# Kernel tuning notes

Measured on AMD Instinct MI355X. Metric: run time of the kernel, lower is better.

## Reference

```python
import jax, jax.numpy as jnp
import numpy as np

# Model dims (match init_kwargs)
D_MODEL = 1024
D_INNER = 2048
D_STATE = 16
D_CONV = 4
DT_RANK = 64
H = 8                      # num_heads
P = D_INNER // H           # head_dim = 256
DT_MIN, DT_MAX = 1e-4, 1.0
BATCH, SEQ = 2, 4096
TOTAL_OUT = 2 * D_INNER + DT_RANK + 2 * H * D_STATE  # 4416 (no gated delta)
EPS = 1e-6


def _xavier(k, shape):
    fan_out, fan_in = shape
    return jax.random.normal(k, shape, jnp.float32) * np.sqrt(2.0 / (fan_in + fan_out))


def setup_inputs() -> dict:
    key = jax.random.key(0)
    ks = jax.random.split(key, 8)
    x = jax.random.normal(ks[0], (BATCH, SEQ, D_MODEL), jnp.float32)
    W_in = _xavier(ks[1], (TOTAL_OUT, D_MODEL))          # in_proj (no bias)
    W_dt = _xavier(ks[2], (H, DT_RANK))                  # dt_proj (no bias)
    conv_w = jax.random.normal(ks[3], (D_INNER, D_CONV), jnp.float32) * 0.1
    conv_b = jnp.zeros((D_INNER,), jnp.float32)
    # A_log init: log(1..d_state) per head
    A_log = jnp.broadcast_to(jnp.log(jnp.arange(1, D_STATE + 1, dtype=jnp.float32)), (H, D_STATE))
    Dskip = jnp.ones((H, P), jnp.float32)
    # dt_bias = inverse_softplus(dt), dt log-uniform in [dt_min, dt_max]
    dt0 = jnp.exp(jax.random.uniform(ks[4], (H,), jnp.float32)
                  * (np.log(DT_MAX) - np.log(DT_MIN)) + np.log(DT_MIN))
    dt_bias = dt0 + jnp.log(-jnp.expm1(-dt0))
    norm_w = jnp.ones((D_INNER,), jnp.float32)
    W_out = _xavier(ks[5], (D_MODEL, D_INNER))
    W_res = _xavier(ks[6], (D_INNER, D_MODEL))           # residual_proj (d_model != d_inner)
    return dict(x=x, W_in=W_in, W_dt=W_dt, conv_w=conv_w, conv_b=conv_b,
                A_log=A_log, Dskip=Dskip, dt_bias=dt_bias, norm_w=norm_w,
                W_out=W_out, W_res=W_res)


def _causal_dwconv(u, w, b):
    # u: (B,L,C) -> causal depthwise conv along L. w: (C,K), b: (C,)
    lhs = u.transpose(0, 2, 1)               # (B,C,L)
    rhs = w[:, None, :]                      # (C,1,K)
    out = jax.lax.conv_general_dilated(
        lhs, rhs, window_strides=(1,), padding=[(D_CONV - 1, 0)],
        dimension_numbers=('NCH', 'OIH', 'NCH'), feature_group_count=D_INNER)
    return (out + b[None, :, None]).transpose(0, 2, 1)


def reference(x, W_in, W_dt, conv_w, conv_b, A_log, Dskip, dt_bias, norm_w, W_out, W_res):
    Bsz, L, _ = x.shape
    p = x @ W_in.T                                            # (B,L,TOTAL_OUT)
    splits = np.cumsum([D_INNER, D_INNER, DT_RANK, H * D_STATE]).tolist()
    z, u, dt_h, Bf, Cf = jnp.split(p, splits, axis=-1)
    Bp = Bf.reshape(Bsz, L, H, D_STATE)
    Cp = Cf.reshape(Bsz, L, H, D_STATE)
    u = _causal_dwconv(u, conv_w, conv_b)                     # (B,L,D_INNER)
    # dt_prep: softplus(dt_raw + bias) clamped to [dt_min, dt_max]
    dt = jnp.clip(jax.nn.softplus(dt_h @ W_dt.T + dt_bias), DT_MIN, DT_MAX)  # (B,L,H)
    A = -jnp.exp(A_log)                                       # (H,N)
    uh = u.reshape(Bsz, L, H, P)

    def step(h, inp):
        u_t, dt_t, B_t, C_t = inp                             # (B,H,P),(B,H),(B,H,N),(B,H,N)
        dA = jnp.exp(dt_t[..., None] * A)                     # (B,H,N)
        h = h * dA[:, :, None, :] + (dt_t[:, :, None, None] * u_t[..., None]) * B_t[:, :, None, :]
        y_t = jnp.einsum('bhpn,bhn->bhp', h, C_t)
        return h, y_t

    h0 = jnp.zeros((Bsz, H, P, D_STATE), x.dtype)
    xs = (uh.transpose(1, 0, 2, 3), dt.transpose(1, 0, 2),
          Bp.transpose(1, 0, 2, 3), Cp.transpose(1, 0, 2, 3))
    _, ys = jax.lax.scan(step, h0, xs)                        # (L,B,H,P)
    y = ys.transpose(1, 0, 2, 3) + Dskip[None, None] * uh     # skip connection
    y = y.reshape(Bsz, L, D_INNER)

    residual_inner = x @ W_res.T                              # residual_proj
    # fused_out: g = RMSNorm(y * silu(z) + residual) * weight
    g = y * jax.nn.silu(z) + residual_inner
    g = g * jax.lax.rsqrt(jnp.mean(g * g, axis=-1, keepdims=True) + EPS) * norm_w
    return g @ W_out.T
```

## Files before the change

kernel.cpp:

```cpp
#include <hip/hip_runtime.h>
#include <hip/hip_bf16.h>
#include <math.h>

#define DMODEL  1024
#define DINNER  2048
#define DSTATE  16
#define DCONV   4
#define DTRANK  64
#define NH      8
#define PH      256
#define TOTOUT  4416
#define NPAD    4608
#define NTOT    6656
#define MB_ROWS 4096
#define LC      64
#define NCB     (MB_ROWS/LC)

typedef __attribute__((ext_vector_type(8))) short bf16x8;
typedef __attribute__((ext_vector_type(4))) float f32x4;

__device__ inline unsigned cvt2bf(float lo, float hi) {
    unsigned r;
    asm("v_cvt_pk_bf16_f32 %0, %1, %2" : "=v"(r) : "v"(lo), "v"(hi));
    return r;
}
__device__ inline ushort f2bf(float v) { return (ushort)(cvt2bf(v, v) & 0xffffu); }
__device__ inline float bf2f(ushort u) {
    union { unsigned u; float f; } w; w.u = (unsigned)u << 16; return w.f;
}
__device__ inline void gload16(const ushort* g, ushort* l) {
    __builtin_amdgcn_global_load_lds((const __attribute__((address_space(1))) unsigned*)(const void*)g,
                                     (__attribute__((address_space(3))) unsigned*)(void*)l, 16, 0, 0);
}

__global__ __launch_bounds__(256) void cvt_bf(const float* __restrict__ s,
                                              ushort* __restrict__ d) {
    size_t i = ((size_t)blockIdx.x * 256 + threadIdx.x) * 8;
    float4 v0 = *(const float4*)(s + i);
    float4 v1 = *(const float4*)(s + i + 4);
    uint4 o;
    o.x = cvt2bf(v0.x, v0.y); o.y = cvt2bf(v0.z, v0.w);
    o.z = cvt2bf(v1.x, v1.y); o.w = cvt2bf(v1.z, v1.w);
    *(uint4*)(d + i) = o;
}

__global__ __launch_bounds__(256) void cvt_weights(const float* __restrict__ W_in,
                                                   const float* __restrict__ W_res,
                                                   const float* __restrict__ W_out,
                                                   ushort* __restrict__ dst) {
    const size_t E0 = (size_t)TOTOUT * DMODEL;
    const size_t E1 = (size_t)NPAD * DMODEL;
    const size_t E2 = (size_t)NTOT * DMODEL;
    size_t i = ((size_t)blockIdx.x * 256 + threadIdx.x) * 8;
    float4 v0, v1;
    if (i < E1) {
        if (i < E0) { v0 = *(const float4*)(W_in + i); v1 = *(const float4*)(W_in + i + 4); }
        else { v0 = make_float4(0.f,0.f,0.f,0.f); v1 = v0; }
    } else if (i < E2) {
        size_t o = i - E1; v0 = *(const float4*)(W_res + o); v1 = *(const float4*)(W_res + o + 4);
    } else {
        size_t o = i - E2; v0 = *(const float4*)(W_out + o); v1 = *(const float4*)(W_out + o + 4);
    }
    uint4 o;
    o.x = cvt2bf(v0.x, v0.y); o.y = cvt2bf(v0.z, v0.w);
    o.z = cvt2bf(v1.x, v1.y); o.w = cvt2bf(v1.z, v1.w);
    *(uint4*)(dst + i) = o;
}

__global__ __launch_bounds__(512, 2) void gemm_big(const ushort* __restrict__ A,
                                                   const ushort* __restrict__ W,
                                                   ushort* __restrict__ Zb,
                                                   ushort* __restrict__ Ub,
                                                   float* __restrict__ DBCp,
                                                   ushort* __restrict__ RESb,
                                                   int ntx, int K) {
    __shared__ __align__(16) ushort L[3 * 16384];
    const int nwg  = gridDim.x;
    const int orig = blockIdx.x;
    const int swz  = (orig & 7) * (nwg >> 3) + (orig >> 3);
    const int bx = swz % ntx, by = swz / ntx;
    const int row0 = by * 256, col0 = bx * 256;

    const int t    = threadIdx.x;
    const int lane = t & 63, w = t >> 6;
    const int wr   = w >> 2, wc = w & 3;
    const int l15  = lane & 15, l4 = lane >> 4;

    const int r0g = t >> 2, s0g = t & 3;
    const int r1g = r0g + 128;
    const int rr0 = r0g ^ ((r0g >> 3) & 1), cc0 = s0g ^ ((r0g >> 1) & 3);
    const int rr1 = r1g ^ ((r1g >> 3) & 1), cc1 = s0g ^ ((r1g >> 1) & 3);
    const ushort* sA0 = A + (size_t)(row0 + rr0) * K + cc0 * 8;
    const ushort* sA1 = A + (size_t)(row0 + rr1) * K + cc1 * 8;
    const ushort* sB0 = W + (size_t)(col0 + rr0) * K + cc0 * 8;
    const ushort* sB1 = W + (size_t)(col0 + rr1) * K + cc1 * 8;

    int offA[8], offB[4];
    #pragma unroll
    for (int mi = 0; mi < 8; mi++) {
        int r = wr * 128 + mi * 16 + l15;
        offA[mi] = (r * 32 + l4 * 8) ^ (((r >> 1) & 7) << 3);
    }
    #pragma unroll
    for (int ni = 0; ni < 4; ni++) {
        int r = wc * 64 + ni * 16 + l15;
        offB[ni] = 8192 + ((r * 32 + l4 * 8) ^ (((r >> 1) & 7) << 3));
    }

    f32x4 acc[8][4];
    #pragma unroll
    for (int i = 0; i < 8; i++)
        #pragma unroll
        for (int j = 0; j < 4; j++)
            acc[i][j] = (f32x4){0.f, 0.f, 0.f, 0.f};

    const int KT = K >> 5;
    gload16(sA0,      &L[t * 8]);
    gload16(sA1,      &L[4096 + t * 8]);
    gload16(sB0,      &L[8192 + t * 8]);
    gload16(sB1,      &L[12288 + t * 8]);
    gload16(sA0 + 32, &L[16384 + t * 8]);
    gload16(sA1 + 32, &L[16384 + 4096 + t * 8]);
    gload16(sB0 + 32, &L[16384 + 8192 + t * 8]);
    gload16(sB1 + 32, &L[16384 + 12288 + t * 8]);
    asm volatile("s_waitcnt vmcnt(4)" ::: "memory");
    __builtin_amdgcn_sched_barrier(0);
    __builtin_amdgcn_s_barrier();
    __builtin_amdgcn_sched_barrier(0);

    for (int kt = 0; kt < KT; ++kt) {
        const bool pre = (kt + 2) < KT;
        if (pre) {
            ushort* bp2 = &L[((kt + 2) % 3) * 16384];
            const int ko = (kt + 2) << 5;
            gload16(sA0 + ko, bp2 + t * 8);
            gload16(sA1 + ko, bp2 + 4096 + t * 8);
            gload16(sB0 + ko, bp2 + 8192 + t * 8);
            gload16(sB1 + ko, bp2 + 12288 + t * 8);
        }
        const ushort* bp = &L[(kt % 3) * 16384];
        bf16x8 af[8], bw[4];
        #pragma unroll
        for (int mi = 0; mi < 8; mi++) af[mi] = *(const bf16x8*)(bp + offA[mi]);
        #pragma unroll
        for (int ni = 0; ni < 4; ni++) bw[ni] = *(const bf16x8*)(bp + offB[ni]);
        __builtin_amdgcn_s_setprio(1);
        #pragma unroll
        for (int mi = 0; mi < 8; mi++)
            #pragma unroll
            for (int ni = 0; ni < 4; ni++)
                acc[mi][ni] = __builtin_amdgcn_mfma_f32_16x16x32_bf16(af[mi], bw[ni], acc[mi][ni], 0, 0, 0);
        __builtin_amdgcn_s_setprio(0);
        if (pre) { asm volatile("s_waitcnt vmcnt(4)" ::: "memory"); }
        else     { asm volatile("s_waitcnt vmcnt(0)" ::: "memory"); }
        __builtin_amdgcn_sched_barrier(0);
        __builtin_amdgcn_s_barrier();
        __builtin_amdgcn_sched_barrier(0);
    }

    #pragma unroll
    for (int mi = 0; mi < 8; mi++) {
        #pragma unroll
        for (int ni = 0; ni < 4; ni++) {
            #pragma unroll
            for (int r = 0; r < 4; r++) {
                const int row = row0 + wr * 128 + mi * 16 + l4 * 4 + r;
                const int col = col0 + wc * 64 + ni * 16 + l15;
                const float v = acc[mi][ni][r];
                if (col0 < DINNER) {
                    Zb[(size_t)row * DINNER + col] = f2bf(v);
                } else if (col0 < 2 * DINNER) {
                    Ub[(size_t)row * DINNER + (col - DINNER)] = f2bf(v);
                } else if (col0 < NPAD) {
                    if (col < TOTOUT)
                        DBCp[(size_t)row * 320 + (col - 2 * DINNER)] = v;
                } else {
                    RESb[(size_t)row * DINNER + (col - NPAD)] = f2bf(v);
                }
            }
        }
    }
}

__global__ __launch_bounds__(512) void gemm_out(const ushort* __restrict__ A,
                                                const ushort* __restrict__ W,
                                                float* __restrict__ C0,
                                                int ntx, int K, int ldc) {
    __shared__ __align__(16) ushort L[3 * 12288];
    const int nwg  = gridDim.x;
    const int orig = blockIdx.x;
    const int swz  = (orig & 7) * (nwg >> 3) + (orig >> 3);
    const int bx = swz % ntx, by = swz / ntx;
    const int row0 = by * 256, col0 = bx * 128;

    const int t    = threadIdx.x;
    const int lane = t & 63, w = t >> 6;
    const int wr   = w >> 1, wc = w & 1;
    const int l15  = lane & 15, l4 = lane >> 4;

    const int r0g = t >> 2, s0g = t & 3;
    const int r1g = r0g + 128;
    const int rr0 = r0g ^ ((r0g >> 3) & 1), cc0 = s0g ^ ((r0g >> 1) & 3);
    const int rr1 = r1g ^ ((r1g >> 3) & 1), cc1 = s0g ^ ((r1g >> 1) & 3);
    const ushort* sA0 = A + (size_t)(row0 + rr0) * K + cc0 * 8;
    const ushort* sA1 = A + (size_t)(row0 + rr1) * K + cc1 * 8;
    const ushort* sB0 = W + (size_t)(col0 + rr0) * K + cc0 * 8;

    int offA[4], offB[4];
    #pragma unroll
    for (int mi = 0; mi < 4; mi++) {
        int r = wr * 64 + mi * 16 + l15;
        offA[mi] = (r * 32 + l4 * 8) ^ (((r >> 1) & 7) << 3);
    }
    #pragma unroll
    for (int ni = 0; ni < 4; ni++) {
        int r = wc * 64 + ni * 16 + l15;
        offB[ni] = 8192 + ((r * 32 + l4 * 8) ^ (((r >> 1) & 7) << 3));
    }

    f32x4 acc[4][4];
    #pragma unroll
    for (int i = 0; i < 4; i++)
        #pragma unroll
        for (int j = 0; j < 4; j++)
            acc[i][j] = (f32x4){0.f, 0.f, 0.f, 0.f};

    const int KT = K >> 5;
    gload16(sA0,      &L[t * 8]);
    gload16(sA1,      &L[4096 + t * 8]);
    gload16(sB0,      &L[8192 + t * 8]);
    gload16(sA0 + 32, &L[12288 + t * 8]);
    gload16(sA1 + 32, &L[12288 + 4096 + t * 8]);
    gload16(sB0 + 32, &L[12288 + 8192 + t * 8]);
    asm volatile("s_waitcnt vmcnt(3)" ::: "memory");
    __builtin_amdgcn_sched_barrier(0);
    __builtin_amdgcn_s_barrier();
    __builtin_amdgcn_sched_barrier(0);

    for (int kt = 0; kt < KT; ++kt) {
        const bool pre = (kt + 2) < KT;
        if (pre) {
            ushort* bp2 = &L[((kt + 2) % 3) * 12288];
            const int ko = (kt + 2) << 5;
            gload16(sA0 + ko, bp2 + t * 8);
            gload16(sA1 + ko, bp2 + 4096 + t * 8);
            gload16(sB0 + ko, bp2 + 8192 + t * 8);
        }
        const ushort* bp = &L[(kt % 3) * 12288];
        bf16x8 af[4], bw[4];
        #pragma unroll
        for (int mi = 0; mi < 4; mi++) af[mi] = *(const bf16x8*)(bp + offA[mi]);
        #pragma unroll
        for (int ni = 0; ni < 4; ni++) bw[ni] = *(const bf16x8*)(bp + offB[ni]);
        __builtin_amdgcn_s_setprio(1);
        #pragma unroll
        for (int mi = 0; mi < 4; mi++)
            #pragma unroll
            for (int ni = 0; ni < 4; ni++)
                acc[mi][ni] = __builtin_amdgcn_mfma_f32_16x16x32_bf16(af[mi], bw[ni], acc[mi][ni], 0, 0, 0);
        __builtin_amdgcn_s_setprio(0);
        if (pre) { asm volatile("s_waitcnt vmcnt(3)" ::: "memory"); }
        else     { asm volatile("s_waitcnt vmcnt(0)" ::: "memory"); }
        __builtin_amdgcn_sched_barrier(0);
        __builtin_amdgcn_s_barrier();
        __builtin_amdgcn_sched_barrier(0);
    }

    #pragma unroll
    for (int mi = 0; mi < 4; mi++)
        #pragma unroll
        for (int ni = 0; ni < 4; ni++)
            #pragma unroll
            for (int r = 0; r < 4; r++) {
                const int row = row0 + wr * 64 + mi * 16 + l4 * 4 + r;
                const int col = col0 + wc * 64 + ni * 16 + l15;
                C0[(size_t)row * ldc + col] = acc[mi][ni][r];
            }
}

__global__ __launch_bounds__(256) void dt_kernel(const float* __restrict__ DBC,
                                                 const float* __restrict__ W_dt,
                                                 const float* __restrict__ dt_bias,
                                                 const float* __restrict__ A_log,
                                                 float* __restrict__ dt,
                                                 float* __restrict__ dA) {
    int idx = blockIdx.x * blockDim.x + threadIdx.x;
    int h = idx % NH;
    int tr = idx / NH;
    const float* row = DBC + (size_t)tr * 320;
    float acc = dt_bias[h];
    #pragma unroll
    for (int r = 0; r < DTRANK; r++) acc = fmaf(row[r], W_dt[h * DTRANK + r], acc);
    float sp = acc > 20.f ? acc : log1pf(expf(acc));
    sp = fminf(fmaxf(sp, 1e-4f), 1.0f);
    dt[idx] = sp;
    #pragma unroll
    for (int n = 0; n < DSTATE; n++)
        dA[(size_t)idx * DSTATE + n] = expf(sp * (-expf(A_log[h * DSTATE + n])));
}

__global__ __launch_bounds__(256) void scan_local(const ushort* __restrict__ Ub,
                                                  const float* __restrict__ DBC,
                                                  const float* __restrict__ dt_,
                                                  const float* __restrict__ dA_,
                                                  const float* __restrict__ cw,
                                                  const float* __restrict__ cb,
                                                  float* __restrict__ hloc,
                                                  float* __restrict__ Pc) {
    const int c = blockIdx.x, h = blockIdx.y;
    const int pidx = threadIdx.x;
    const int ch = h * PH + pidx;
    const int t0 = c * LC;
    __shared__ float sdA[LC][DSTATE];
    __shared__ float sdB[LC][DSTATE];
    const int st = pidx >> 4, sn = pidx & 15;
    #pragma unroll
    for (int j = 0; j < 4; j++) {
        int tt = st + j * 16;
        size_t trow = (size_t)(t0 + tt);
        float dv = dt_[trow * NH + h];
        sdA[tt][sn] = dA_[(trow * NH + h) * DSTATE + sn];
        sdB[tt][sn] = dv * DBC[trow * 320 + 64 + h * DSTATE + sn];
    }
    const float w0 = cw[ch * 4], w1 = cw[ch * 4 + 1], w2 = cw[ch * 4 + 2], w3 = cw[ch * 4 + 3];
    const float bia = cb[ch];
    const int bs = (c / NCB) * MB_ROWS;
    float um3 = (t0 - 3 >= bs) ? bf2f(Ub[(size_t)(t0 - 3) * DINNER + ch]) : 0.f;
    float um2 = (t0 - 2 >= bs) ? bf2f(Ub[(size_t)(t0 - 2) * DINNER + ch]) : 0.f;
    float um1 = (t0 - 1 >= bs) ? bf2f(Ub[(size_t)(t0 - 1) * DINNER + ch]) : 0.f;
    __syncthreads();

    float hst[DSTATE] = {};
    for (int t = 0; t < LC; t++) {
        float u0 = bf2f(Ub[(size_t)(t0 + t) * DINNER + ch]);
        float up = fmaf(w3, u0, fmaf(w2, um1, fmaf(w1, um2, fmaf(w0, um3, bia))));
        um3 = um2; um2 = um1; um1 = u0;
        #pragma unroll
        for (int n = 0; n < DSTATE; n++)
            hst[n] = fmaf(hst[n], sdA[t][n], up * sdB[t][n]);
    }
    float* hl = hloc + (((size_t)c * NH + h) * PH + pidx) * DSTATE;
    #pragma unroll
    for (int n = 0; n < DSTATE; n++) hl[n] = hst[n];

    if (pidx < DSTATE) {
        float pr = 1.f;
        for (int t = 0; t < LC; t++) pr *= sdA[t][pidx];
        Pc[((size_t)c * NH + h) * DSTATE + pidx] = pr;
    }
}

__global__ __launch_bounds__(256) void scan_carry(const float* __restrict__ hloc,
                                                  const float* __restrict__ Pc,
                                                  float* __restrict__ Hent) {
    int g = blockIdx.x * 256 + threadIdx.x;
    int b = g >> 15;
    int r = g & 32767;
    int h = r >> 12;
    int inner = r & 4095;
    int n = r & 15;
    float carry = 0.f;
    for (int i = 0; i < NCB; i++) {
        int c = b * NCB + i;
        size_t idx = ((size_t)c * NH + h) * (PH * DSTATE) + inner;
        Hent[idx] = carry;
        carry = fmaf(Pc[((size_t)c * NH + h) * DSTATE + n], carry, hloc[idx]);
    }
}

__global__ __launch_bounds__(256) void scan_out(const ushort* __restrict__ Zb,
                                                const ushort* __restrict__ Ub,
                                                const ushort* __restrict__ RESb,
                                                ushort* __restrict__ Yb,
                                                const float* __restrict__ DBC,
                                                const float* __restrict__ dt_,
                                                const float* __restrict__ dA_,
                                                const float* __restrict__ cw,
                                                const float* __restrict__ cb,
                                                const float* __restrict__ Dskip,
                                                const float* __restrict__ Hent) {
    const int c = blockIdx.x, h = blockIdx.y;
    const int pidx = threadIdx.x;
    const int ch = h * PH + pidx;
    const int t0 = c * LC;
    __shared__ float sdA[LC][DSTATE];
    __shared__ float sdB[LC][DSTATE];
    __shared__ float sC [LC][DSTATE];
    const int st = pidx >> 4, sn = pidx & 15;
    #pragma unroll
    for (int j = 0; j < 4; j++) {
        int tt = st + j * 16;
        size_t trow = (size_t)(t0 + tt);
        float dv = dt_[trow * NH + h];
        sdA[tt][sn] = dA_[(trow * NH + h) * DSTATE + sn];
        sdB[tt][sn] = dv * DBC[trow * 320 + 64 + h * DSTATE + sn];
        sC [tt][sn] =      DBC[trow * 320 + 192 + h * DSTATE + sn];
    }
    const float w0 = cw[ch * 4], w1 = cw[ch * 4 + 1], w2 = cw[ch * 4 + 2], w3 = cw[ch * 4 + 3];
    const float bia = cb[ch];
    const int bs = (c / NCB) * MB_ROWS;
    float um3 = (t0 - 3 >= bs) ? bf2f(Ub[(size_t)(t0 - 3) * DINNER + ch]) : 0.f;
    float um2 = (t0 - 2 >= bs) ? bf2f(Ub[(size_t)(t0 - 2) * DINNER + ch]) : 0.f;
    float um1 = (t0 - 1 >= bs) ? bf2f(Ub[(size_t)(t0 - 1) * DINNER + ch]) : 0.f;
    const float dsk = Dskip[ch];
    float hst[DSTATE];
    const float* he = Hent + (((size_t)c * NH + h) * PH + pidx) * DSTATE;
    #pragma unroll
    for (int n = 0; n < DSTATE; n++) hst[n] = he[n];
    __syncthreads();

    for (int t = 0; t < LC; t++) {
        size_t off = (size_t)(t0 + t) * DINNER + ch;
        float u0 = bf2f(Ub[off]);
        float up = fmaf(w3, u0, fmaf(w2, um1, fmaf(w1, um2, fmaf(w0, um3, bia))));
        um3 = um2; um2 = um1; um1 = u0;
        float a0 = 0.f, a1 = 0.f, a2 = 0.f, a3 = 0.f;
        #pragma unroll
        for (int n = 0; n < 4; n++) {
            hst[n +  0] = fmaf(hst[n +  0], sdA[t][n +  0], up * sdB[t][n +  0]);
            hst[n +  4] = fmaf(hst[n +  4], sdA[t][n +  4], up * sdB[t][n +  4]);
            hst[n +  8] = fmaf(hst[n +  8], sdA[t][n +  8], up * sdB[t][n +  8]);
            hst[n + 12] = fmaf(hst[n + 12], sdA[t][n + 12], up * sdB[t][n + 12]);
            a0 = fmaf(hst[n +  0], sC[t][n +  0], a0);
            a1 = fmaf(hst[n +  4], sC[t][n +  4], a1);
            a2 = fmaf(hst[n +  8], sC[t][n +  8], a2);
            a3 = fmaf(hst[n + 12], sC[t][n + 12], a3);
        }
        float yv = ((a0 + a1) + (a2 + a3)) + dsk * up;
        float zv = bf2f(Zb[off]);
        float sil = zv / (1.f + expf(-zv));
        Yb[off] = f2bf(fmaf(yv, sil, bf2f(RESb[off])));
    }
}

__global__ __launch_bounds__(256) void rmsnorm_bf(const ushort* __restrict__ Yb,
                                                  const float* __restrict__ norm_w,
                                                  ushort* __restrict__ Gb) {
    const int row = blockIdx.x;
    const ushort* r = Yb + (size_t)row * DINNER;
    const int c0 = threadIdx.x * 8;
    uint4 packed = *(const uint4*)(r + c0);
    float v[8];
    v[0] = bf2f((ushort)(packed.x & 0xffff)); v[1] = bf2f((ushort)(packed.x >> 16));
    v[2] = bf2f((ushort)(packed.y & 0xffff)); v[3] = bf2f((ushort)(packed.y >> 16));
    v[4] = bf2f((ushort)(packed.z & 0xffff)); v[5] = bf2f((ushort)(packed.z >> 16));
    v[6] = bf2f((ushort)(packed.w & 0xffff)); v[7] = bf2f((ushort)(packed.w >> 16));
    float ss = 0.f;
    #pragma unroll
    for (int i = 0; i < 8; i++) ss = fmaf(v[i], v[i], ss);
    #pragma unroll
    for (int off = 32; off > 0; off >>= 1) ss += __shfl_down(ss, off);
    __shared__ float red[4];
    if ((threadIdx.x & 63) == 0) red[threadIdx.x >> 6] = ss;
    __syncthreads();
    float tot = red[0] + red[1] + red[2] + red[3];
    float inv = rsqrtf(tot / (float)DINNER + 1e-6f);
    float4 w0 = *(const float4*)(norm_w + c0);
    float4 w1 = *(const float4*)(norm_w + c0 + 4);
    uint4 o;
    o.x = cvt2bf(v[0] * inv * w0.x, v[1] * inv * w0.y);
    o.y = cvt2bf(v[2] * inv * w0.z, v[3] * inv * w0.w);
    o.z = cvt2bf(v[4] * inv * w1.x, v[5] * inv * w1.y);
    o.w = cvt2bf(v[6] * inv * w1.z, v[7] * inv * w1.w);
    *(uint4*)(Gb + (size_t)row * DINNER + c0) = o;
}

struct Lay {
    float *DBC, *DT, *DA, *PC, *HLOC, *HENT;
    ushort *YB, *ZB, *UB, *RESB, *XBF, *WB;
    size_t total;
};
static Lay mk_layout(char* base, int Mr) {
    size_t o = 0;
    auto take = [&](size_t bytes) { char* p = base + o; o = (o + bytes + 255) & ~(size_t)255; return p; };
    Lay l;
    l.YB   = (ushort*)take((size_t)Mr * 2048 * 2);
    l.DBC  = (float*) take((size_t)Mr * 320 * 4);
    l.DT   = (float*) take((size_t)Mr * 8 * 4);
    l.DA   = (float*) take((size_t)Mr * 128 * 4);
    l.PC   = (float*) take((size_t)(Mr / 64) * NH * DSTATE * 4);
    l.HLOC = (float*) take((size_t)Mr * 512 * 4);
    l.HENT = (float*) take((size_t)Mr * 512 * 4);
    l.ZB   = (ushort*)take((size_t)Mr * 2048 * 2);
    l.UB   = (ushort*)take((size_t)Mr * 2048 * 2);
    l.RESB = (ushort*)take((size_t)Mr * 2048 * 2);
    l.XBF  = (ushort*)take((size_t)8192 * 1024 * 2);
    l.WB   = (ushort*)take(((size_t)NTOT * 1024 + (size_t)1024 * 2048) * 2);
    l.total = o;
    return l;
}

extern "C" void kernel_launch(void* const* d_in, const int* in_sizes, int n_in,
                              void* d_out, int out_size, void* d_ws, size_t ws_size,
                              hipStream_t stream) {
    const float* x       = (const float*)d_in[0];
    const float* W_in    = (const float*)d_in[1];
    const float* W_dt    = (const float*)d_in[2];
    const float* conv_w  = (const float*)d_in[3];
    const float* conv_b  = (const float*)d_in[4];
    const float* A_log   = (const float*)d_in[5];
    const float* Dskip   = (const float*)d_in[6];
    const float* dt_bias = (const float*)d_in[7];
    const float* norm_w  = (const float*)d_in[8];
    const float* W_out   = (const float*)d_in[9];
    const float* W_res   = (const float*)d_in[10];
    float* out = (float*)d_out;

    Lay probe = mk_layout(nullptr, 2 * MB_ROWS);
    const bool fat = ws_size >= probe.total;
    const int Mr = fat ? 2 * MB_ROWS : MB_ROWS;
    const int npass = fat ? 1 : 2;
    const int nbc = fat ? 2 : 1;
    Lay l = mk_layout((char*)d_ws, Mr);

    ushort* wcat = l.WB;
    ushort* wotb = wcat + (size_t)NTOT * 1024;
    ushort* Gb   = l.ZB;

    cvt_weights<<<((NTOT * 1024 + 2048 * 1024) / 8) / 256, 256, 0, stream>>>(W_in, W_res, W_out, l.WB);
    cvt_bf<<<(2 * MB_ROWS * DMODEL / 8) / 256, 256, 0, stream>>>(x, l.XBF);

    for (int b = 0; b < npass; b++) {
        const ushort* xb = l.XBF + (size_t)b * MB_ROWS * DMODEL;
        float* outb = out + (size_t)b * MB_ROWS * DMODEL;
        const int nty = Mr / 256;

        gemm_big<<<26 * nty, 512, 0, stream>>>(xb, wcat, l.ZB, l.UB, l.DBC, l.RESB, 26, DMODEL);
        dt_kernel<<<(Mr * NH) / 256, 256, 0, stream>>>(l.DBC, W_dt, dt_bias, A_log, l.DT, l.DA);
        scan_local<<<dim3(Mr / LC, NH), 256, 0, stream>>>(l.UB, l.DBC, l.DT, l.DA, conv_w, conv_b, l.HLOC, l.PC);
        scan_carry<<<nbc * 128, 256, 0, stream>>>(l.HLOC, l.PC, l.HENT);
        scan_out<<<dim3(Mr / LC, NH), 256, 0, stream>>>(l.ZB, l.UB, l.RESB, l.YB, l.DBC, l.DT, l.DA,
                                                        conv_w, conv_b, Dskip, l.HENT);
        rmsnorm_bf<<<Mr, 256, 0, stream>>>(l.YB, norm_w, Gb);
        gemm_out<<<8 * nty, 512, 0, stream>>>(Gb, wotb, outb, 8, DINNER, DMODEL);
    }
}
```

Baseline: 326.4 us.

## Restructure big GEMM to BK=64 double-buffered pipeline with interleaved staged loads

Replaces the triple-buffered BK=32 main loop of the input-projection GEMM with a double-buffered BK=64 loop. Each K-step is split into four sub-phases, and each phase issues one quarter of the next tile's global loads before its MFMA block. The LDS layout changes to 16-element half-rows with a simple XOR swizzle, and the LDS footprint grows from 96KB to 128KB. The aim is to halve barrier count per K and overlap global loads with MFMA more finely. The cost is higher LDS use, which may limit 2 blocks per CU, and possible bank conflicts under the new swizzle.

```diff
diff --git a/kernel.cpp b/kernel.cpp
--- a/kernel.cpp
+++ b/kernel.cpp
@@ -67,14 +67,14 @@
     *(uint4*)(dst + i) = o;
 }
 
-__global__ __launch_bounds__(512, 2) void gemm_big(const ushort* __restrict__ A,
-                                                   const ushort* __restrict__ W,
-                                                   ushort* __restrict__ Zb,
-                                                   ushort* __restrict__ Ub,
-                                                   float* __restrict__ DBCp,
-                                                   ushort* __restrict__ RESb,
-                                                   int ntx, int K) {
-    __shared__ __align__(16) ushort L[3 * 16384];
+__global__ __launch_bounds__(512, 2) void gemm_big8(const ushort* __restrict__ A,
+                                                    const ushort* __restrict__ W,
+                                                    ushort* __restrict__ Zb,
+                                                    ushort* __restrict__ Ub,
+                                                    float* __restrict__ DBCp,
+                                                    ushort* __restrict__ RESb,
+                                                    int ntx, int K) {
+    __shared__ __align__(16) ushort L[2 * 32768];
     const int nwg  = gridDim.x;
     const int orig = blockIdx.x;
     const int swz  = (orig & 7) * (nwg >> 3) + (orig >> 3);
@@ -86,25 +86,26 @@
     const int wr   = w >> 2, wc = w & 3;
     const int l15  = lane & 15, l4 = lane >> 4;
 
-    const int r0g = t >> 2, s0g = t & 3;
-    const int r1g = r0g + 128;
-    const int rr0 = r0g ^ ((r0g >> 3) & 1), cc0 = s0g ^ ((r0g >> 1) & 3);
-    const int rr1 = r1g ^ ((r1g >> 3) & 1), cc1 = s0g ^ ((r1g >> 1) & 3);
-    const ushort* sA0 = A + (size_t)(row0 + rr0) * K + cc0 * 8;
-    const ushort* sA1 = A + (size_t)(row0 + rr1) * K + cc1 * 8;
-    const ushort* sB0 = W + (size_t)(col0 + rr0) * K + cc0 * 8;
-    const ushort* sB1 = W + (size_t)(col0 + rr1) * K + cc1 * 8;
+    const int r  = t >> 1, hp = t & 1;
+    const int kb = hp ^ ((r >> 2) & 1);
+    const ushort* sA = A + (size_t)(row0 + r) * K + kb * 8;
+    const ushort* sB = W + (size_t)(col0 + r) * K + kb * 8;
+    const int ldst = t * 8;
+
+#define STG(d, p, ko) do { \
+    gload16(sA + (ko) + (p) * 16, &L[(d) * 32768 + (p) * 4096 + ldst]); \
+    gload16(sB + (ko) + (p) * 16, &L[(d) * 32768 + 16384 + (p) * 4096 + ldst]); } while (0)
 
     int offA[8], offB[4];
     #pragma unroll
     for (int mi = 0; mi < 8; mi++) {
-        int r = wr * 128 + mi * 16 + l15;
-        offA[mi] = (r * 32 + l4 * 8) ^ (((r >> 1) & 7) << 3);
+        int R = wr * 128 + mi * 16 + l15;
+        offA[mi] = (l4 >> 1) * 4096 + R * 16 + (((l4 & 1) ^ ((R >> 2) & 1)) * 8);
     }
     #pragma unroll
     for (int ni = 0; ni < 4; ni++) {
-        int r = wc * 64 + ni * 16 + l15;
-        offB[ni] = 8192 + ((r * 32 + l4 * 8) ^ (((r >> 1) & 7) << 3));
+        int R = wc * 64 + ni * 16 + l15;
+        offB[ni] = 16384 + (l4 >> 1) * 4096 + R * 16 + (((l4 & 1) ^ ((R >> 2) & 1)) * 8);
     }
 
     f32x4 acc[8][4];
@@ -114,59 +115,135 @@
         for (int j = 0; j < 4; j++)
             acc[i][j] = (f32x4){0.f, 0.f, 0.f, 0.f};
 
-    const int KT = K >> 5;
-    gload16(sA0,      &L[t * 8]);
-    gload16(sA1,      &L[4096 + t * 8]);
-    gload16(sB0,      &L[8192 + t * 8]);
-    gload16(sB1,      &L[12288 + t * 8]);
-    gload16(sA0 + 32, &L[16384 + t * 8]);
-    gload16(sA1 + 32, &L[16384 + 4096 + t * 8]);
-    gload16(sB0 + 32, &L[16384 + 8192 + t * 8]);
-    gload16(sB1 + 32, &L[16384 + 12288 + t * 8]);
+    const int KT = K >> 6;
+    STG(0, 0, 0); STG(0, 1, 0); STG(0, 2, 0); STG(0, 3, 0);
     asm volatile("s_waitcnt vmcnt(4)" ::: "memory");
     __builtin_amdgcn_sched_barrier(0);
     __builtin_amdgcn_s_barrier();
     __builtin_amdgcn_sched_barrier(0);
 
     for (int kt = 0; kt < KT; ++kt) {
-        const bool pre = (kt + 2) < KT;
-        if (pre) {
-            ushort* bp2 = &L[((kt + 2) % 3) * 16384];
-            const int ko = (kt + 2) << 5;
-            gload16(sA0 + ko, bp2 + t * 8);
-            gload16(sA1 + ko, bp2 + 4096 + t * 8);
-            gload16(sB0 + ko, bp2 + 8192 + t * 8);
-            gload16(sB1 + ko, bp2 + 12288 + t * 8);
-        }
-        const ushort* bp = &L[(kt % 3) * 16384];
-        bf16x8 af[8], bw[4];
-        #pragma unroll
-        for (int mi = 0; mi < 8; mi++) af[mi] = *(const bf16x8*)(bp + offA[mi]);
-        #pragma unroll
-        for (int ni = 0; ni < 4; ni++) bw[ni] = *(const bf16x8*)(bp + offB[ni]);
+        const int d = kt & 1;
+        const bool pre = (kt + 1) < KT;
+        const int ko = (kt + 1) << 6;
+        const ushort* Lp = &L[d * 32768];
+        bf16x8 af0, af1, af2, af3, bw0, bw1, bw2, bw3;
+
+        if (pre) STG(d ^ 1, 0, ko);
+        bw0 = *(const bf16x8*)(Lp + offB[0]); bw1 = *(const bf16x8*)(Lp + offB[1]);
+        bw2 = *(const bf16x8*)(Lp + offB[2]); bw3 = *(const bf16x8*)(Lp + offB[3]);
+        af0 = *(const bf16x8*)(Lp + offA[0]); af1 = *(const bf16x8*)(Lp + offA[1]);
+        af2 = *(const bf16x8*)(Lp + offA[2]); af3 = *(const bf16x8*)(Lp + offA[3]);
         __builtin_amdgcn_s_setprio(1);
-        #pragma unroll
-        for (int mi = 0; mi < 8; mi++)
-            #pragma unroll
-            for (int ni = 0; ni < 4; ni++)
-                acc[mi][ni] = __builtin_amdgcn_mfma_f32_16x16x32_bf16(af[mi], bw[ni], acc[mi][ni], 0, 0, 0);
+        acc[0][0] = __builtin_amdgcn_mfma_f32_16x16x32_bf16(af0, bw0, acc[0][0], 0, 0, 0);
+        acc[0][1] = __builtin_amdgcn_mfma_f32_16x16x32_bf16(af0, bw1, acc[0][1], 0, 0, 0);
+        acc[0][2] = __builtin_amdgcn_mfma_f32_16x16x32_bf16(af0, bw2, acc[0][2], 0, 0, 0);
+        acc[0][3] = __builtin_amdgcn_mfma_f32_16x16x32_bf16(af0, bw3, acc[0][3], 0, 0, 0);
+        acc[1][0] = __builtin_amdgcn_mfma_f32_16x16x32_bf16(af1, bw0, acc[1][0], 0, 0, 0);
+        acc[1][1] = __builtin_amdgcn_mfma_f32_16x16x32_bf16(af1, bw1, acc[1][1], 0, 0, 0);
+        acc[1][2] = __builtin_amdgcn_mfma_f32_16x16x32_bf16(af1, bw2, acc[1][2], 0, 0, 0);
+        acc[1][3] = __builtin_amdgcn_mfma_f32_16x16x32_bf16(af1, bw3, acc[1][3], 0, 0, 0);
+        acc[2][0] = __builtin_amdgcn_mfma_f32_16x16x32_bf16(af2, bw0, acc[2][0], 0, 0, 0);
+        acc[2][1] = __builtin_amdgcn_mfma_f32_16x16x32_bf16(af2, bw1, acc[2][1], 0, 0, 0);
+        acc[2][2] = __builtin_amdgcn_mfma_f32_16x16x32_bf16(af2, bw2, acc[2][2], 0, 0, 0);
+        acc[2][3] = __builtin_amdgcn_mfma_f32_16x16x32_bf16(af2, bw3, acc[2][3], 0, 0, 0);
+        acc[3][0] = __builtin_amdgcn_mfma_f32_16x16x32_bf16(af3, bw0, acc[3][0], 0, 0, 0);
+        acc[3][1] = __builtin_amdgcn_mfma_f32_16x16x32_bf16(af3, bw1, acc[3][1], 0, 0, 0);
+        acc[3][2] = __builtin_amdgcn_mfma_f32_16x16x32_bf16(af3, bw2, acc[3][2], 0, 0, 0);
+        acc[3][3] = __builtin_amdgcn_mfma_f32_16x16x32_bf16(af3, bw3, acc[3][3], 0, 0, 0);
         __builtin_amdgcn_s_setprio(0);
+
+        if (pre) STG(d ^ 1, 1, ko);
+        af0 = *(const bf16x8*)(Lp + offA[4]); af1 = *(const bf16x8*)(Lp + offA[5]);
+        af2 = *(const bf16x8*)(Lp + offA[6]); af3 = *(const bf16x8*)(Lp + offA[7]);
+        __builtin_amdgcn_s_setprio(1);
+        acc[4][0] = __builtin_amdgcn_mfma_f32_16x16x32_bf16(af0, bw0, acc[4][0], 0, 0, 0);
+        acc[4][1] = __builtin_amdgcn_mfma_f32_16x16x32_bf16(af0, bw1, acc[4][1], 0, 0, 0);
+        acc[4][2] = __builtin_amdgcn_mfma_f32_16x16x32_bf16(af0, bw2, acc[4][2], 0, 0, 0);
+        acc[4][3] = __builtin_amdgcn_mfma_f32_16x16x32_bf16(af0, bw3, acc[4][3], 0, 0, 0);
+        acc[5][0] = __builtin_amdgcn_mfma_f32_16x16x32_bf16(af1, bw0, acc[5][0], 0, 0, 0);
+        acc[5][1] = __builtin_amdgcn_mfma_f32_16x16x32_bf16(af1, bw1, acc[5][1], 0, 0, 0);
+        acc[5][2] = __builtin_amdgcn_mfma_f32_16x16x32_bf16(af1, bw2, acc[5][2], 0, 0, 0);
+        acc[5][3] = __builtin_amdgcn_mfma_f32_16x16x32_bf16(af1, bw3, acc[5][3], 0, 0, 0);
+        acc[6][0] = __builtin_amdgcn_mfma_f32_16x16x32_bf16(af2, bw0, acc[6][0], 0, 0, 0);
+        acc[6][1] = __builtin_amdgcn_mfma_f32_16x16x32_bf16(af2, bw1, acc[6][1], 0, 0, 0);
+        acc[6][2] = __builtin_amdgcn_mfma_f32_16x16x32_bf16(af2, bw2, acc[6][2], 0, 0, 0);
+        acc[6][3] = __builtin_amdgcn_mfma_f32_16x16x32_bf16(af2, bw3, acc[6][3], 0, 0, 0);
+        acc[7][0] = __builtin_amdgcn_mfma_f32_16x16x32_bf16(af3, bw0, acc[7][0], 0, 0, 0);
+        acc[7][1] = __builtin_amdgcn_mfma_f32_16x16x32_bf16(af3, bw1, acc[7][1], 0, 0, 0);
+        acc[7][2] = __builtin_amdgcn_mfma_f32_16x16x32_bf16(af3, bw2, acc[7][2], 0, 0, 0);
+        acc[7][3] = __builtin_amdgcn_mfma_f32_16x16x32_bf16(af3, bw3, acc[7][3], 0, 0, 0);
+        __builtin_amdgcn_s_setprio(0);
+
         if (pre) { asm volatile("s_waitcnt vmcnt(4)" ::: "memory"); }
         else     { asm volatile("s_waitcnt vmcnt(0)" ::: "memory"); }
         __builtin_amdgcn_sched_barrier(0);
         __builtin_amdgcn_s_barrier();
         __builtin_amdgcn_sched_barrier(0);
-    }
+
+        if (pre) STG(d ^ 1, 2, ko);
+        bw0 = *(const bf16x8*)(Lp + 8192 + offB[0]); bw1 = *(const bf16x8*)(Lp + 8192 + offB[1]);
+        bw2 = *(const bf16x8*)(Lp + 8192 + offB[2]); bw3 = *(const bf16x8*)(Lp + 8192 + offB[3]);
+        af0 = *(const bf16x8*)(Lp + 8192 + offA[0]); af1 = *(const bf16x8*)(Lp + 8192 + offA[1]);
+        af2 = *(const bf16x8*)(Lp + 8192 + offA[2]); af3 = *(const bf16x8*)(Lp + 8192 + offA[3]);
+        __builtin_amdgcn_s_setprio(1);
+        acc[0][0] = __builtin_amdgcn_mfma_f32_16x16x32_bf16(af0, bw0, acc[0][0], 0, 0, 0);
+        acc[0][1] = __builtin_amdgcn_mfma_f32_16x16x32_bf16(af0, bw1, acc[0][1], 0, 0, 0);
+        acc[0][2] = __builtin_amdgcn_mfma_f32_16x16x32_bf16(af0, bw2, acc[0][2], 0, 0, 0);
+        acc[0][3] = __builtin_amdgcn_mfma_f32_16x16x32_bf16(af0, bw3, acc[0][3], 0, 0, 0);
+        acc[1][0] = __builtin_amdgcn_mfma_f32_16x16x32_bf16(af1, bw0, acc[1][0], 0, 0, 0);
+        acc[1][1] = __builtin_amdgcn_mfma_f32_16x16x32_bf16(af1, bw1, acc[1][1], 0, 0, 0);
+        acc[1][2] = __builtin_amdgcn_mfma_f32_16x16x32_bf16(af1, bw2, acc[1][2], 0, 0, 0);
+        acc[1][3] = __builtin_amdgcn_mfma_f32_16x16x32_bf16(af1, bw3, acc[1][3], 0, 0, 0);
+        acc[2][0] = __builtin_amdgcn_mfma_f32_16x16x32_bf16(af2, bw0, acc[2][0], 0, 0, 0);
+        acc[2][1] = __builtin_amdgcn_mfma_f32_16x16x32_bf16(af2, bw1, acc[2][1], 0, 0, 0);
+        acc[2][2] = __builtin_amdgcn_mfma_f32_16x16x32_bf16(af2, bw2, acc[2][2], 0, 0, 0);
+        acc[2][3] = __builtin_amdgcn_mfma_f32_16x16x32_bf16(af2, bw3, acc[2][3], 0, 0, 0);
+        acc[3][0] = __builtin_amdgcn_mfma_f32_16x16x32_bf16(af3, bw0, acc[3][0], 0, 0, 0);
+        acc[3][1] = __builtin_amdgcn_mfma_f32_16x16x32_bf16(af3, bw1, acc[3][1], 0, 0, 0);
+        acc[3][2] = __builtin_amdgcn_mfma_f32_16x16x32_bf16(af3, bw2, acc[3][2], 0, 0, 0);
+        acc[3][3] = __builtin_amdgcn_mfma_f32_16x16x32_bf16(af3, bw3, acc[3][3], 0, 0, 0);
+        __builtin_amdgcn_s_setprio(0);
+
+        if (pre) STG(d ^ 1, 3, ko);
+        af0 = *(const bf16x8*)(Lp + 8192 + offA[4]); af1 = *(const bf16x8*)(Lp + 8192 + offA[5]);
+        af2 = *(const bf16x8*)(Lp + 8192 + offA[6]); af3 = *(const bf16x8*)(Lp + 8192 + offA[7]);
+        __builtin_amdgcn_s_setprio(1);
+        acc[4][0] = __builtin_amdgcn_mfma_f32_16x16x32_bf16(af0, bw0, acc[4][0], 0, 0, 0);
+        acc[4][1] = __builtin_amdgcn_mfma_f32_16x16x32_bf16(af0, bw1, acc[4][1], 0, 0, 0);
+        acc[4][2] = __builtin_amdgcn_mfma_f32_16x16x32_bf16(af0, bw2, acc[4][2], 0, 0, 0);
+        acc[4][3] = __builtin_amdgcn_mfma_f32_16x16x32_bf16(af0, bw3, acc[4][3], 0, 0, 0);
+        acc[5][0] = __builtin_amdgcn_mfma_f32_16x16x32_bf16(af1, bw0, acc[5][0], 0, 0, 0);
+        acc[5][1] = __builtin_amdgcn_mfma_f32_16x16x32_bf16(af1, bw1, acc[5][1], 0, 0, 0);
+        acc[5][2] = __builtin_amdgcn_mfma_f32_16x16x32_bf16(af1, bw2, acc[5][2], 0, 0, 0);
+        acc[5][3] = __builtin_amdgcn_mfma_f32_16x16x32_bf16(af1, bw3, acc[5][3], 0, 0, 0);
+        acc[6][0] = __builtin_amdgcn_mfma_f32_16x16x32_bf16(af2, bw0, acc[6][0], 0, 0, 0);
+        acc[6][1] = __builtin_amdgcn_mfma_f32_16x16x32_bf16(af2, bw1, acc[6][1], 0, 0, 0);
+        acc[6][2] = __builtin_amdgcn_mfma_f32_16x16x32_bf16(af2, bw2, acc[6][2], 0, 0, 0);
+        acc[6][3] = __builtin_amdgcn_mfma_f32_16x16x32_bf16(af2, bw3, acc[6][3], 0, 0, 0);
+        acc[7][0] = __builtin_amdgcn_mfma_f32_16x16x32_bf16(af3, bw0, acc[7][0], 0, 0, 0);
+        acc[7][1] = __builtin_amdgcn_mfma_f32_16x16x32_bf16(af3, bw1, acc[7][1], 0, 0, 0);
+        acc[7][2] = __builtin_amdgcn_mfma_f32_16x16x32_bf16(af3, bw2, acc[7][2], 0, 0, 0);
+        acc[7][3] = __builtin_amdgcn_mfma_f32_16x16x32_bf16(af3, bw3, acc[7][3], 0, 0, 0);
+        __builtin_amdgcn_s_setprio(0);
+
+        if (pre) { asm volatile("s_waitcnt vmcnt(4)" ::: "memory"); }
+        else     { asm volatile("s_waitcnt vmcnt(0)" ::: "memory"); }
+        __builtin_amdgcn_sched_barrier(0);
+        __builtin_amdgcn_s_barrier();
+        __builtin_amdgcn_sched_barrier(0);
+    }
+#undef STG
 
     #pragma unroll
     for (int mi = 0; mi < 8; mi++) {
         #pragma unroll
         for (int ni = 0; ni < 4; ni++) {
             #pragma unroll
-            for (int r = 0; r < 4; r++) {
-                const int row = row0 + wr * 128 + mi * 16 + l4 * 4 + r;
+            for (int rr = 0; rr < 4; rr++) {
+                const int row = row0 + wr * 128 + mi * 16 + l4 * 4 + rr;
                 const int col = col0 + wc * 64 + ni * 16 + l15;
-                const float v = acc[mi][ni][r];
+                const float v = acc[mi][ni][rr];
                 if (col0 < DINNER) {
                     Zb[(size_t)row * DINNER + col] = f2bf(v);
                 } else if (col0 < 2 * DINNER) {
@@ -209,13 +286,13 @@
     int offA[4], offB[4];
     #pragma unroll
     for (int mi = 0; mi < 4; mi++) {
-        int r = wr * 64 + mi * 16 + l15;
-        offA[mi] = (r * 32 + l4 * 8) ^ (((r >> 1) & 7) << 3);
+        int rq = wr * 64 + mi * 16 + l15;
+        offA[mi] = (rq * 32 + l4 * 8) ^ (((rq >> 1) & 7) << 3);
     }
     #pragma unroll
     for (int ni = 0; ni < 4; ni++) {
-        int r = wc * 64 + ni * 16 + l15;
-        offB[ni] = 8192 + ((r * 32 + l4 * 8) ^ (((r >> 1) & 7) << 3));
+        int rq = wc * 64 + ni * 16 + l15;
+        offB[ni] = 8192 + ((rq * 32 + l4 * 8) ^ (((rq >> 1) & 7) << 3));
     }
 
     f32x4 acc[4][4];
@@ -271,10 +348,10 @@
         #pragma unroll
         for (int ni = 0; ni < 4; ni++)
             #pragma unroll
-            for (int r = 0; r < 4; r++) {
-                const int row = row0 + wr * 64 + mi * 16 + l4 * 4 + r;
+            for (int rr = 0; rr < 4; rr++) {
+                const int row = row0 + wr * 64 + mi * 16 + l4 * 4 + rr;
                 const int col = col0 + wc * 64 + ni * 16 + l15;
-                C0[(size_t)row * ldc + col] = acc[mi][ni][r];
+                C0[(size_t)row * ldc + col] = acc[mi][ni][rr];
             }
 }
 
@@ -525,7 +602,7 @@
         float* outb = out + (size_t)b * MB_ROWS * DMODEL;
         const int nty = Mr / 256;
 
-        gemm_big<<<26 * nty, 512, 0, stream>>>(xb, wcat, l.ZB, l.UB, l.DBC, l.RESB, 26, DMODEL);
+        gemm_big8<<<26 * nty, 512, 0, stream>>>(xb, wcat, l.ZB, l.UB, l.DBC, l.RESB, 26, DMODEL);
         dt_kernel<<<(Mr * NH) / 256, 256, 0, stream>>>(l.DBC, W_dt, dt_bias, A_log, l.DT, l.DA);
         scan_local<<<dim3(Mr / LC, NH), 256, 0, stream>>>(l.UB, l.DBC, l.DT, l.DA, conv_w, conv_b, l.HLOC, l.PC);
         scan_carry<<<nbc * 128, 256, 0, stream>>>(l.HLOC, l.PC, l.HENT);
```

Result: slower. 336.8 us (+3.2%).
